# Performance work log

Measured on AMD Instinct MI355X. Metric: run time of the kernel, lower is better.

Reference implementation:

```python
import jax, jax.numpy as jnp
import numpy as np

N = 100000
E = 640000
IN_CH = 256
OUT_CH = 64
HID = 2 * OUT_CH  # 128


def setup_inputs() -> dict:
    key = jax.random.key(0)
    ks = jax.random.split(key, 8)
    x = jax.random.normal(ks[0], (N, IN_CH), dtype=jnp.float32)
    edge_index = jax.random.randint(ks[1], (2, E), 0, N, dtype=jnp.int32)
    s = 1.0 / np.sqrt(IN_CH)
    W1 = jax.random.uniform(ks[2], (IN_CH, HID), jnp.float32, -s, s)
    b1 = jnp.zeros((HID,), jnp.float32)
    s2 = 1.0 / np.sqrt(HID)
    W_mu = jax.random.uniform(ks[3], (HID, OUT_CH), jnp.float32, -s2, s2)
    b_mu = jnp.zeros((OUT_CH,), jnp.float32)
    W_ls = jax.random.uniform(ks[4], (HID, OUT_CH), jnp.float32, -s2, s2)
    b_ls = jnp.zeros((OUT_CH,), jnp.float32)
    return {"x": x, "W1": W1, "b1": b1, "W_mu": W_mu, "b_mu": b_mu,
            "W_ls": W_ls, "b_ls": b_ls, "edge_index": edge_index}


def _gcn_norm(edge_index, n_nodes):
    # PyG GCNConv default: add self-loops, symmetric normalization D^-1/2 A D^-1/2
    loops = jnp.arange(n_nodes, dtype=edge_index.dtype)
    src = jnp.concatenate([edge_index[0], loops])
    dst = jnp.concatenate([edge_index[1], loops])
    deg = jax.ops.segment_sum(jnp.ones_like(dst, jnp.float32), dst, num_segments=n_nodes)
    dinv = jnp.where(deg > 0, jax.lax.rsqrt(deg), 0.0)
    norm = dinv[src] * dinv[dst]  # [E+N]
    return src, dst, norm


def _gcn_conv(x, W, b, src, dst, norm, n_nodes):
    h = x @ W                                   # [N, F_out]
    msg = h[src] * norm[:, None]                # [E+N, F_out] gather
    out = jax.ops.segment_sum(msg, dst, num_segments=n_nodes)  # scatter-add
    return out + b


def reference(x, W1, b1, W_mu, b_mu, W_ls, b_ls, edge_index):
    src, dst, norm = _gcn_norm(edge_index, N)
    h = jax.nn.relu(_gcn_conv(x, W1, b1, src, dst, norm, N))
    mu = _gcn_conv(h, W_mu, b_mu, src, dst, norm, N)
    logstd = _gcn_conv(h, W_ls, b_ls, src, dst, norm, N)
    return mu, logstd
```

## Files before the change

kernel.cpp:

```cpp
#include <hip/hip_runtime.h>
#include <math.h>

#define NN 100000
#define EE 640000
#define INCH 256
#define HIDC 128
#define OUTC 64
#define NCHUNK ((NN + 255) / 256)

typedef __attribute__((ext_vector_type(8))) short short8;
typedef __attribute__((ext_vector_type(8))) unsigned short ushort8;
typedef __attribute__((ext_vector_type(4))) float floatx4;

__device__ __forceinline__ short f2bf(float f) {
    unsigned u = __float_as_uint(f);
    u += 0x7fff + ((u >> 16) & 1);
    return (short)(u >> 16);
}

__device__ __forceinline__ float bf2f(unsigned short u) {
    return __uint_as_float(((unsigned)u) << 16);
}

__device__ __forceinline__ unsigned pk2bf(float lo, float hi) {
    unsigned r;
    asm("v_cvt_pk_bf16_f32 %0, %1, %2" : "=v"(r) : "v"(lo), "v"(hi));
    return r;
}

__global__ void k_deg_zero(int* __restrict__ deg) {
    int i = blockIdx.x * 256 + threadIdx.x;
    if (i < NN) deg[i] = 0;
}

__global__ void k_deg_count(const int* __restrict__ dstp, int* __restrict__ deg) {
    int e = blockIdx.x * 256 + threadIdx.x;
    if (e < EE) atomicAdd(&deg[dstp[e]], 1);
}

__global__ __launch_bounds__(256) void k_scan1(const int* __restrict__ deg,
                                               int* __restrict__ partials) {
    int i = blockIdx.x * 256 + threadIdx.x;
    int v = (i < NN) ? deg[i] : 0;
    for (int o = 32; o; o >>= 1) v += __shfl_down(v, o, 64);
    __shared__ int sm[4];
    if ((threadIdx.x & 63) == 0) sm[threadIdx.x >> 6] = v;
    __syncthreads();
    if (threadIdx.x == 0) partials[blockIdx.x] = sm[0] + sm[1] + sm[2] + sm[3];
}

__global__ __launch_bounds__(512) void k_scan2(int* __restrict__ partials) {
    __shared__ int sm[512];
    int t = threadIdx.x;
    int v = (t < NCHUNK) ? partials[t] : 0;
    sm[t] = v;
    __syncthreads();
    for (int o = 1; o < 512; o <<= 1) {
        int add = (t >= o) ? sm[t - o] : 0;
        __syncthreads();
        sm[t] += add;
        __syncthreads();
    }
    if (t < NCHUNK) partials[t] = sm[t] - v;
}

__global__ __launch_bounds__(256) void k_scan3(const int* __restrict__ deg,
                                               const int* __restrict__ partials,
                                               int* __restrict__ row_off,
                                               int* __restrict__ cursor,
                                               float* __restrict__ dinv) {
    int t = threadIdx.x;
    int i = blockIdx.x * 256 + t;
    int v = (i < NN) ? deg[i] : 0;
    __shared__ int sm[256];
    sm[t] = v;
    __syncthreads();
    for (int o = 1; o < 256; o <<= 1) {
        int add = (t >= o) ? sm[t - o] : 0;
        __syncthreads();
        sm[t] += add;
        __syncthreads();
    }
    if (i < NN) {
        int excl = partials[blockIdx.x] + sm[t] - v;
        row_off[i] = excl;
        cursor[i] = excl;
        dinv[i] = rsqrtf((float)(v + 1));
    }
}

__global__ void k_fill(const int* __restrict__ srcp, const int* __restrict__ dstp,
                       int* __restrict__ cursor, int* __restrict__ esrc) {
    int e = blockIdx.x * 256 + threadIdx.x;
    if (e < EE) {
        int d = dstp[e];
        int pos = atomicAdd(&cursor[d], 1);
        esrc[pos] = srcp[e];
    }
}

__global__ void k_prep(const float* __restrict__ W1,
                       const float* __restrict__ Wmu, const float* __restrict__ bmu,
                       const float* __restrict__ Wls, const float* __restrict__ bls,
                       short* __restrict__ wt, short* __restrict__ wct,
                       float* __restrict__ bcat) {
    int i = blockIdx.x * 256 + threadIdx.x;
    if (i < 32768) {
        int n = i >> 8, k = i & 255;
        wt[i] = f2bf(W1[k * HIDC + n]);
    } else if (i < 32768 + 16384) {
        int j = i - 32768;
        int n = j >> 7, k = j & 127;
        float v = (n < OUTC) ? Wmu[k * OUTC + n] : Wls[k * OUTC + (n - OUTC)];
        wct[j] = f2bf(v);
    } else if (i < 32768 + 16384 + 128) {
        int c = i - (32768 + 16384);
        bcat[c] = (c < OUTC) ? bmu[c] : bls[c - OUTC];
    }
}

__global__ __launch_bounds__(256, 1) void k_mgemm1(const float* __restrict__ x,
                                                   const short* __restrict__ wt,
                                                   short* __restrict__ out) {
    int wave = threadIdx.x >> 6;
    int lane = threadIdx.x & 63;
    int rhalf = wave & 1, chalf = wave >> 1;
    int m = lane & 15, quad = lane >> 4;
    int rbase = blockIdx.x * 64 + rhalf * 32;
    int r0c = min(rbase + m, NN - 1);
    int r1c = min(rbase + 16 + m, NN - 1);
    const float* xr0 = x + (size_t)r0c * INCH + quad * 8;
    const float* xr1 = x + (size_t)r1c * INCH + quad * 8;

    float4 px0[16], px1[16];
#pragma unroll
    for (int c = 0; c < 8; c++) {
        px0[2 * c]     = *(const float4*)(xr0 + c * 32);
        px0[2 * c + 1] = *(const float4*)(xr0 + c * 32 + 4);
        px1[2 * c]     = *(const float4*)(xr1 + c * 32);
        px1[2 * c + 1] = *(const float4*)(xr1 + c * 32 + 4);
    }
    __builtin_amdgcn_sched_barrier(0);

    const short* wbase = wt + quad * 8 + (size_t)m * INCH + (size_t)(chalf * 4) * 16 * INCH;
    floatx4 acc0[4], acc1[4];
#pragma unroll
    for (int i = 0; i < 4; i++) { acc0[i] = (floatx4)(0.f); acc1[i] = (floatx4)(0.f); }

#pragma unroll
    for (int k = 0; k < 8; k++) {
        union { short8 s; unsigned u[4]; } a0, a1;
        float4 p;
        p = px0[2 * k];     a0.u[0] = pk2bf(p.x, p.y); a0.u[1] = pk2bf(p.z, p.w);
        p = px0[2 * k + 1]; a0.u[2] = pk2bf(p.x, p.y); a0.u[3] = pk2bf(p.z, p.w);
        p = px1[2 * k];     a1.u[0] = pk2bf(p.x, p.y); a1.u[1] = pk2bf(p.z, p.w);
        p = px1[2 * k + 1]; a1.u[2] = pk2bf(p.x, p.y); a1.u[3] = pk2bf(p.z, p.w);
        const short* wq = wbase + k * 32;
#pragma unroll
        for (int nt = 0; nt < 4; nt++) {
            short8 b = *(const short8*)(wq + (size_t)nt * 16 * INCH);
            acc0[nt] = __builtin_amdgcn_mfma_f32_16x16x32_bf16(a0.s, b, acc0[nt], 0, 0, 0);
            acc1[nt] = __builtin_amdgcn_mfma_f32_16x16x32_bf16(a1.s, b, acc1[nt], 0, 0, 0);
        }
    }

    int rs0 = rbase + quad * 4;
    int rs1 = rbase + 16 + quad * 4;
#pragma unroll
    for (int nt = 0; nt < 4; nt++) {
        int c = (chalf * 4 + nt) * 16 + m;
#pragma unroll
        for (int r = 0; r < 4; r++) {
            int rr = rs0 + r;
            if (rr < NN) out[(size_t)rr * HIDC + c] = f2bf(acc0[nt][r]);
            int rr2 = rs1 + r;
            if (rr2 < NN) out[(size_t)rr2 * HIDC + c] = f2bf(acc1[nt][r]);
        }
    }
}

__global__ __launch_bounds__(256, 1) void k_mgemm2(const short* __restrict__ agg,
                                                   const short* __restrict__ wct,
                                                   const float* __restrict__ bcat,
                                                   float* __restrict__ out) {
    int wave = threadIdx.x >> 6;
    int lane = threadIdx.x & 63;
    int rhalf = wave & 1, chalf = wave >> 1;
    int m = lane & 15, quad = lane >> 4;
    int rbase = blockIdx.x * 64 + rhalf * 32;
    int r0c = min(rbase + m, NN - 1);
    int r1c = min(rbase + 16 + m, NN - 1);
    const short* ar0 = agg + (size_t)r0c * HIDC + quad * 8;
    const short* ar1 = agg + (size_t)r1c * HIDC + quad * 8;

    short8 pa0[4], pa1[4];
#pragma unroll
    for (int c = 0; c < 4; c++) {
        pa0[c] = *(const short8*)(ar0 + c * 32);
        pa1[c] = *(const short8*)(ar1 + c * 32);
    }
    __builtin_amdgcn_sched_barrier(0);

    const short* wbase = wct + quad * 8 + (size_t)m * HIDC + (size_t)(chalf * 4) * 16 * HIDC;
    floatx4 acc0[4], acc1[4];
#pragma unroll
    for (int i = 0; i < 4; i++) { acc0[i] = (floatx4)(0.f); acc1[i] = (floatx4)(0.f); }
#pragma unroll
    for (int k = 0; k < 4; k++) {
        const short* wq = wbase + k * 32;
#pragma unroll
        for (int nt = 0; nt < 4; nt++) {
            short8 b = *(const short8*)(wq + (size_t)nt * 16 * HIDC);
            acc0[nt] = __builtin_amdgcn_mfma_f32_16x16x32_bf16(pa0[k], b, acc0[nt], 0, 0, 0);
            acc1[nt] = __builtin_amdgcn_mfma_f32_16x16x32_bf16(pa1[k], b, acc1[nt], 0, 0, 0);
        }
    }
    int rs0 = rbase + quad * 4;
    int rs1 = rbase + 16 + quad * 4;
#pragma unroll
    for (int nt = 0; nt < 4; nt++) {
        int c = (chalf * 4 + nt) * 16 + m;
        float bv = bcat[c];
        float* obase = (c < OUTC) ? (out + c) : (out + (size_t)NN * OUTC + (c - OUTC));
#pragma unroll
        for (int r = 0; r < 4; r++) {
            int rr = rs0 + r;
            if (rr < NN) obase[(size_t)rr * OUTC] = acc0[nt][r] + bv;
            int rr2 = rs1 + r;
            if (rr2 < NN) obase[(size_t)rr2 * OUTC] = acc1[nt][r] + bv;
        }
    }
}

template <bool RELU>
__global__ __launch_bounds__(256) void k_gather(const short* __restrict__ feat,
                                                const int* __restrict__ esrc,
                                                const int* __restrict__ row_off,
                                                const int* __restrict__ deg,
                                                const float* __restrict__ dinv,
                                                const float* __restrict__ bias,
                                                short* __restrict__ out) {
    int gid = blockIdx.x * 256 + threadIdx.x;
    int d = gid >> 4;
    int l = threadIdx.x & 15;
    if (d >= NN) return;
    const ushort8* fp = (const ushort8*)feat;
    float dd = dinv[d];
    float sw = dd * dd;
    ushort8 sv = fp[(size_t)d * 16 + l];
    float acc[8];
#pragma unroll
    for (int i = 0; i < 8; i++) acc[i] = bf2f(sv[i]) * sw;
    int off = row_off[d];
    int cnt = deg[d];
    for (int base = 0; base < cnt; base += 16) {
        int mm = min(16, cnt - base);
        int sj = (l < mm) ? esrc[off + base + l] : 0;
        float dj = (l < mm) ? dinv[sj] : 0.f;
        int j = 0;
        for (; j + 4 <= mm; j += 4) {
            int s0 = __shfl(sj, j + 0, 16);
            int s1 = __shfl(sj, j + 1, 16);
            int s2 = __shfl(sj, j + 2, 16);
            int s3 = __shfl(sj, j + 3, 16);
            float n0 = __shfl(dj, j + 0, 16) * dd;
            float n1 = __shfl(dj, j + 1, 16) * dd;
            float n2 = __shfl(dj, j + 2, 16) * dd;
            float n3 = __shfl(dj, j + 3, 16) * dd;
            ushort8 v0 = fp[(size_t)s0 * 16 + l];
            ushort8 v1 = fp[(size_t)s1 * 16 + l];
            ushort8 v2 = fp[(size_t)s2 * 16 + l];
            ushort8 v3 = fp[(size_t)s3 * 16 + l];
#pragma unroll
            for (int i = 0; i < 8; i++) acc[i] = fmaf(bf2f(v0[i]), n0, acc[i]);
#pragma unroll
            for (int i = 0; i < 8; i++) acc[i] = fmaf(bf2f(v1[i]), n1, acc[i]);
#pragma unroll
            for (int i = 0; i < 8; i++) acc[i] = fmaf(bf2f(v2[i]), n2, acc[i]);
#pragma unroll
            for (int i = 0; i < 8; i++) acc[i] = fmaf(bf2f(v3[i]), n3, acc[i]);
        }
        if (j + 2 <= mm) {
            int s0 = __shfl(sj, j + 0, 16);
            int s1 = __shfl(sj, j + 1, 16);
            float n0 = __shfl(dj, j + 0, 16) * dd;
            float n1 = __shfl(dj, j + 1, 16) * dd;
            ushort8 v0 = fp[(size_t)s0 * 16 + l];
            ushort8 v1 = fp[(size_t)s1 * 16 + l];
#pragma unroll
            for (int i = 0; i < 8; i++) acc[i] = fmaf(bf2f(v0[i]), n0, acc[i]);
#pragma unroll
            for (int i = 0; i < 8; i++) acc[i] = fmaf(bf2f(v1[i]), n1, acc[i]);
            j += 2;
        }
        if (j < mm) {
            int s0 = __shfl(sj, j, 16);
            float n0 = __shfl(dj, j, 16) * dd;
            ushort8 v0 = fp[(size_t)s0 * 16 + l];
#pragma unroll
            for (int i = 0; i < 8; i++) acc[i] = fmaf(bf2f(v0[i]), n0, acc[i]);
        }
    }
    if (RELU) {
        float4 b0 = *(const float4*)(bias + l * 8);
        float4 b1 = *(const float4*)(bias + l * 8 + 4);
        acc[0] = fmaxf(acc[0] + b0.x, 0.f);
        acc[1] = fmaxf(acc[1] + b0.y, 0.f);
        acc[2] = fmaxf(acc[2] + b0.z, 0.f);
        acc[3] = fmaxf(acc[3] + b0.w, 0.f);
        acc[4] = fmaxf(acc[4] + b1.x, 0.f);
        acc[5] = fmaxf(acc[5] + b1.y, 0.f);
        acc[6] = fmaxf(acc[6] + b1.z, 0.f);
        acc[7] = fmaxf(acc[7] + b1.w, 0.f);
    }
    ushort8 o;
#pragma unroll
    for (int i = 0; i < 8; i++) o[i] = (unsigned short)f2bf(acc[i]);
    ((ushort8*)out)[(size_t)d * 16 + l] = o;
}

extern "C" void kernel_launch(void* const* d_in, const int* in_sizes, int n_in,
                              void* d_out, int out_size, void* d_ws, size_t ws_size,
                              hipStream_t stream) {
    const float* x   = (const float*)d_in[0];
    const float* W1  = (const float*)d_in[1];
    const float* b1  = (const float*)d_in[2];
    const float* Wmu = (const float*)d_in[3];
    const float* bmu = (const float*)d_in[4];
    const float* Wls = (const float*)d_in[5];
    const float* bls = (const float*)d_in[6];
    const int*   ei  = (const int*)d_in[7];
    const int* srcp = ei;
    const int* dstp = ei + EE;

    float* out = (float*)d_out;

    char* wsb = (char*)d_ws;
    short* bufA    = (short*)wsb;
    short* bufH    = bufA + (size_t)NN * HIDC;
    int*   deg     = (int*)(bufH + (size_t)NN * HIDC);
    int*   row_off = deg + NN;
    int*   cursor  = row_off + NN;
    float* dinv    = (float*)(cursor + NN);
    int*   esrc    = (int*)(dinv + NN);
    int*   partials = esrc + EE;
    short* wt      = (short*)(partials + NCHUNK + 1);
    short* wct     = wt + 128 * 256;
    float* bcat    = (float*)(wct + 128 * 128);

    const int nb_n = (NN + 255) / 256;
    const int nb_e = (EE + 255) / 256;
    const int nb_g = (NN * 16) / 256;
    const int nb_m = (NN + 63) / 64;

    k_deg_zero<<<nb_n, 256, 0, stream>>>(deg);
    k_deg_count<<<nb_e, 256, 0, stream>>>(dstp, deg);
    k_scan1<<<NCHUNK, 256, 0, stream>>>(deg, partials);
    k_scan2<<<1, 512, 0, stream>>>(partials);
    k_scan3<<<NCHUNK, 256, 0, stream>>>(deg, partials, row_off, cursor, dinv);
    k_fill<<<nb_e, 256, 0, stream>>>(srcp, dstp, cursor, esrc);
    k_prep<<<193, 256, 0, stream>>>(W1, Wmu, bmu, Wls, bls, wt, wct, bcat);

    k_mgemm1<<<nb_m, 256, 0, stream>>>(x, wt, bufA);
    k_gather<true><<<nb_g, 256, 0, stream>>>(bufA, esrc, row_off, deg, dinv, b1, bufH);

    k_gather<false><<<nb_g, 256, 0, stream>>>(bufH, esrc, row_off, deg, dinv, nullptr, bufA);
    k_mgemm2<<<nb_m, 256, 0, stream>>>(bufA, wct, bcat, out);
}
```

Before: 371.6 us.

## Stage x tile into LDS via async global_load_lds with XOR swizzle in first GEMM

The first GEMM now copies the 64x256 fp32 x tile straight into shared memory with global_load_lds, using an XOR swizzle to avoid bank conflicts. It also changes the wave decomposition so each wave owns 32 output columns across all 64 rows, holding its weight fragments in registers. Before, each wave loaded its own x rows into registers and half the waves reloaded the same rows. The aim is coalesced, shared loads of x and two blocks per CU. The cost is a 64KB LDS tile, which may limit occupancy, plus correctness risk in the swizzle indexing and the async-copy lane mapping.

```diff
diff --git a/kernel.cpp b/kernel.cpp
--- a/kernel.cpp
+++ b/kernel.cpp
@@ -26,6 +26,13 @@
     unsigned r;
     asm("v_cvt_pk_bf16_f32 %0, %1, %2" : "=v"(r) : "v"(lo), "v"(hi));
     return r;
+}
+
+__device__ __forceinline__ void async_copy16(const void* g, void* l) {
+    __builtin_amdgcn_global_load_lds(
+        (const __attribute__((address_space(1))) unsigned int*)g,
+        (__attribute__((address_space(3))) unsigned int*)l,
+        16, 0, 0);
 }
 
 __global__ void k_deg_zero(int* __restrict__ deg) {
@@ -119,62 +126,70 @@
     }
 }
 
-__global__ __launch_bounds__(256, 1) void k_mgemm1(const float* __restrict__ x,
+__global__ __launch_bounds__(256, 2) void k_mgemm1(const float* __restrict__ x,
                                                    const short* __restrict__ wt,
                                                    short* __restrict__ out) {
+    __shared__ __align__(16) float xs[64 * 256];
     int wave = threadIdx.x >> 6;
     int lane = threadIdx.x & 63;
-    int rhalf = wave & 1, chalf = wave >> 1;
     int m = lane & 15, quad = lane >> 4;
-    int rbase = blockIdx.x * 64 + rhalf * 32;
-    int r0c = min(rbase + m, NN - 1);
-    int r1c = min(rbase + 16 + m, NN - 1);
-    const float* xr0 = x + (size_t)r0c * INCH + quad * 8;
-    const float* xr1 = x + (size_t)r1c * INCH + quad * 8;
-
-    float4 px0[16], px1[16];
-#pragma unroll
-    for (int c = 0; c < 8; c++) {
-        px0[2 * c]     = *(const float4*)(xr0 + c * 32);
-        px0[2 * c + 1] = *(const float4*)(xr0 + c * 32 + 4);
-        px1[2 * c]     = *(const float4*)(xr1 + c * 32);
-        px1[2 * c + 1] = *(const float4*)(xr1 + c * 32 + 4);
-    }
-    __builtin_amdgcn_sched_barrier(0);
-
-    const short* wbase = wt + quad * 8 + (size_t)m * INCH + (size_t)(chalf * 4) * 16 * INCH;
-    floatx4 acc0[4], acc1[4];
-#pragma unroll
-    for (int i = 0; i < 4; i++) { acc0[i] = (floatx4)(0.f); acc1[i] = (floatx4)(0.f); }
-
-#pragma unroll
-    for (int k = 0; k < 8; k++) {
-        union { short8 s; unsigned u[4]; } a0, a1;
-        float4 p;
-        p = px0[2 * k];     a0.u[0] = pk2bf(p.x, p.y); a0.u[1] = pk2bf(p.z, p.w);
-        p = px0[2 * k + 1]; a0.u[2] = pk2bf(p.x, p.y); a0.u[3] = pk2bf(p.z, p.w);
-        p = px1[2 * k];     a1.u[0] = pk2bf(p.x, p.y); a1.u[1] = pk2bf(p.z, p.w);
-        p = px1[2 * k + 1]; a1.u[2] = pk2bf(p.x, p.y); a1.u[3] = pk2bf(p.z, p.w);
-        const short* wq = wbase + k * 32;
-#pragma unroll
-        for (int nt = 0; nt < 4; nt++) {
-            short8 b = *(const short8*)(wq + (size_t)nt * 16 * INCH);
-            acc0[nt] = __builtin_amdgcn_mfma_f32_16x16x32_bf16(a0.s, b, acc0[nt], 0, 0, 0);
-            acc1[nt] = __builtin_amdgcn_mfma_f32_16x16x32_bf16(a1.s, b, acc1[nt], 0, 0, 0);
-        }
-    }
-
-    int rs0 = rbase + quad * 4;
-    int rs1 = rbase + 16 + quad * 4;
-#pragma unroll
-    for (int nt = 0; nt < 4; nt++) {
-        int c = (chalf * 4 + nt) * 16 + m;
-#pragma unroll
-        for (int r = 0; r < 4; r++) {
-            int rr = rs0 + r;
-            if (rr < NN) out[(size_t)rr * HIDC + c] = f2bf(acc0[nt][r]);
-            int rr2 = rs1 + r;
-            if (rr2 < NN) out[(size_t)rr2 * HIDC + c] = f2bf(acc1[nt][r]);
+    int rbase = blockIdx.x * 64;
+
+#pragma unroll
+    for (int i = 0; i < 16; i++) {
+        int r = wave * 16 + i;
+        int grow = rbase + r;
+        if (grow >= NN) grow = NN - 1;
+        const float* gsrc = x + (size_t)grow * INCH + ((lane ^ (r & 7)) << 2);
+        float* ldst = xs + r * INCH;
+        async_copy16(gsrc, ldst);
+    }
+
+    short8 bfr[2][8];
+#pragma unroll
+    for (int ct = 0; ct < 2; ct++)
+#pragma unroll
+        for (int k0 = 0; k0 < 8; k0++)
+            bfr[ct][k0] = *(const short8*)(wt + (size_t)(wave * 32 + ct * 16 + m) * INCH
+                                              + k0 * 32 + quad * 8);
+
+    asm volatile("s_waitcnt vmcnt(0)" ::: "memory");
+    __syncthreads();
+
+    floatx4 acc[4][2];
+#pragma unroll
+    for (int rt = 0; rt < 4; rt++) { acc[rt][0] = (floatx4)(0.f); acc[rt][1] = (floatx4)(0.f); }
+
+#pragma unroll
+    for (int k0 = 0; k0 < 8; k0++) {
+        int cbase = k0 * 8 + (quad << 1);
+#pragma unroll
+        for (int rt = 0; rt < 4; rt++) {
+            int r = rt * 16 + m;
+            int e = m & 7;
+            const float* p0 = xs + r * INCH + (((cbase) ^ e) << 2);
+            const float* p1 = xs + r * INCH + (((cbase + 1) ^ e) << 2);
+            float4 f0 = *(const float4*)p0;
+            float4 f1 = *(const float4*)p1;
+            union { short8 s; unsigned u[4]; } a;
+            a.u[0] = pk2bf(f0.x, f0.y); a.u[1] = pk2bf(f0.z, f0.w);
+            a.u[2] = pk2bf(f1.x, f1.y); a.u[3] = pk2bf(f1.z, f1.w);
+            acc[rt][0] = __builtin_amdgcn_mfma_f32_16x16x32_bf16(a.s, bfr[0][k0], acc[rt][0], 0, 0, 0);
+            acc[rt][1] = __builtin_amdgcn_mfma_f32_16x16x32_bf16(a.s, bfr[1][k0], acc[rt][1], 0, 0, 0);
+        }
+    }
+
+#pragma unroll
+    for (int rt = 0; rt < 4; rt++) {
+        int rs = rbase + rt * 16 + quad * 4;
+#pragma unroll
+        for (int ct = 0; ct < 2; ct++) {
+            int c = wave * 32 + ct * 16 + m;
+#pragma unroll
+            for (int r = 0; r < 4; r++) {
+                int rr = rs + r;
+                if (rr < NN) out[(size_t)rr * HIDC + c] = f2bf(acc[rt][ct][r]);
+            }
         }
     }
 }
```

Measured after the change: 350.0 us. 5.8% less time.
